# Optimization experiments

Measured on AMD Instinct MI355X. Metric: run time of the kernel, lower is better.

## Reference

```python
import jax, jax.numpy as jnp
import numpy as np

V = 50000   # words_num
D = 128     # embedding_dim
B = 2048    # batch
P = 20      # max Huffman path length


def setup_inputs() -> dict:
    key = jax.random.key(0)
    k1, k2, k3, k4, k5 = jax.random.split(key, 5)
    inputs_vector = jax.random.uniform(k1, (B, V), dtype=jnp.float32)
    path_nodes_indices = jax.random.randint(k2, (B, P), 0, V)
    huffman_codes = jax.random.randint(k3, (B, P), 0, 2).astype(jnp.float32)
    mask = jnp.ones((B, P), dtype=jnp.float32)
    # learned params, torch nn.Linear weight layout [out, in], kaiming-uniform-ish scale
    W_emb = jax.random.uniform(k4, (D, V), dtype=jnp.float32, minval=-1.0, maxval=1.0) / np.sqrt(V)
    W_cls = jax.random.uniform(k5, (V, D), dtype=jnp.float32, minval=-1.0, maxval=1.0) / np.sqrt(D)
    return {
        "inputs_vector": inputs_vector,
        "W_emb": W_emb,
        "W_cls": W_cls,
        "path_nodes_indices": path_nodes_indices,
        "huffman_codes": huffman_codes,
        "mask": mask,
    }


def _bce_with_logits(logits, targets):
    # numerically stable, elementwise (reduction='none')
    return jnp.maximum(logits, 0.0) - logits * targets + jnp.log1p(jnp.exp(-jnp.abs(logits)))


def reference(inputs_vector, W_emb, W_cls, path_nodes_indices, huffman_codes, mask):
    x = inputs_vector @ W_emb.T              # [B, D]  embedding Linear (no bias)
    logits_full = x @ W_cls.T                # [B, V]  full-vocab cls matmul (as in source)
    logits = jnp.take_along_axis(logits_full, path_nodes_indices, axis=1)  # [B, P]
    loss = _bce_with_logits(logits, huffman_codes)  # [B, P]
    masked_loss = loss * mask
    per_sample = masked_loss.sum(axis=-1) / mask.sum(axis=-1)  # [B]
    return per_sample.mean()
```

## Files before the change

kernel.cpp:

```cpp
#include <hip/hip_runtime.h>
#include <hip/hip_bf16.h>

#define V 50000
#define D 128
#define B 2048
#define P 20

#define BM 128
#define BK 64
#define LDK 72
#define NSPLIT 48
#define KC 1056
#define VPAD (NSPLIT * KC)
#define NMT (B / BM)

typedef float  f32x4  __attribute__((ext_vector_type(4)));
typedef short  bf16x8 __attribute__((ext_vector_type(8)));
typedef unsigned int uint4v __attribute__((ext_vector_type(4)));
typedef unsigned int uint2v __attribute__((ext_vector_type(2)));

__device__ __forceinline__ unsigned int pk2(float a, float b) {
    return (__float_as_uint(b) & 0xFFFF0000u) | (__float_as_uint(a) >> 16);
}
__device__ __forceinline__ unsigned short f2bf(float f) {
    unsigned int u = __float_as_uint(f);
    return (unsigned short)((u + 0x7FFFu + ((u >> 16) & 1u)) >> 16);
}

__global__ __launch_bounds__(256)
void w2v_wcast(const float* __restrict__ Wemb, unsigned short* __restrict__ Wb) {
    const size_t t = (size_t)blockIdx.x * 256 + threadIdx.x;
    const size_t n = (size_t)D * VPAD / 8;
    if (t >= n) return;
    const size_t base = t * 8;
    const int d = (int)(base / VPAD);
    const int k = (int)(base % VPAD);
    uint4v u = {0u, 0u, 0u, 0u};
    if (k + 8 <= V) {
        const f32x4* src = reinterpret_cast<const f32x4*>(Wemb + (size_t)d * V + k);
        f32x4 v0 = src[0], v1 = src[1];
        u.x = pk2(v0[0], v0[1]); u.y = pk2(v0[2], v0[3]);
        u.z = pk2(v1[0], v1[1]); u.w = pk2(v1[2], v1[3]);
    }
    *reinterpret_cast<uint4v*>(Wb + (size_t)d * VPAD + k) = u;
}

template<int FAST>
__global__ __launch_bounds__(256, 3)
void w2v_gemm(const float* __restrict__ Ain, const void* __restrict__ Wsrc,
              void* __restrict__ part) {
    __shared__ unsigned short Sm[2 * BM * LDK];
    unsigned short* As = Sm;
    unsigned short* Ws = Sm + BM * LDK;

    const int i   = blockIdx.x;
    const int xcd = i & 7;
    const int q   = i >> 3;
    const int s   = xcd * 6 + (q >> 4);
    const int mt  = q & 15;
    const int m0  = mt * BM;
    const int k0  = s * KC;
    const int k1  = (k0 + KC < V) ? (k0 + KC) : V;
    const int nsteps = (k1 - k0 + 63) >> 6;

    const int tid  = threadIdx.x;
    const int lane = tid & 63;
    const int wid  = tid >> 6;
    const int w32  = wid * 32;
    const int fr   = lane & 15;
    const int kg4  = lane >> 4;

    f32x4 acc[2][8] = {};

    const unsigned short* Wb = (const unsigned short*)Wsrc;
    const float*          Wf = (const float*)Wsrc;

    for (int t = 0; t < nsteps; ++t) {
        const int ks = k0 + t * 64;

#pragma unroll
        for (int it = 0; it < 8; ++it) {
            const int slot = tid + it * 256;
            const int row  = slot >> 4;
            const int kv   = slot & 15;
            const int kg   = ks + kv * 4;
            f32x4 v = {0.f, 0.f, 0.f, 0.f};
            if (kg + 4 <= k1)
                v = *reinterpret_cast<const f32x4*>(Ain + (size_t)(m0 + row) * V + kg);
            uint2v u;
            u.x = pk2(v[0], v[1]);
            u.y = pk2(v[2], v[3]);
            *reinterpret_cast<uint2v*>(&As[row * LDK + kv * 4]) = u;
        }
#pragma unroll
        for (int it = 0; it < 4; ++it) {
            const int slot = tid + it * 256;
            const int d    = slot >> 3;
            const int c8   = slot & 7;
            const int kg   = ks + c8 * 8;
            uint4v u;
            if (FAST) {
                u = *reinterpret_cast<const uint4v*>(Wb + (size_t)d * VPAD + kg);
            } else {
                u.x = 0u; u.y = 0u; u.z = 0u; u.w = 0u;
                if (kg + 8 <= V) {
                    const f32x4* sp = reinterpret_cast<const f32x4*>(Wf + (size_t)d * V + kg);
                    f32x4 v0 = sp[0], v1 = sp[1];
                    u.x = pk2(v0[0], v0[1]); u.y = pk2(v0[2], v0[3]);
                    u.z = pk2(v1[0], v1[1]); u.w = pk2(v1[2], v1[3]);
                }
            }
            *reinterpret_cast<uint4v*>(&Ws[d * LDK + c8 * 8]) = u;
        }
        __syncthreads();

#pragma unroll
        for (int kk = 0; kk < BK; kk += 32) {
            const int kfo = kk + kg4 * 8;
            bf16x8 af[2];
#pragma unroll
            for (int m = 0; m < 2; ++m)
                af[m] = *reinterpret_cast<const bf16x8*>(&As[(w32 + m * 16 + fr) * LDK + kfo]);
#pragma unroll
            for (int n = 0; n < 8; ++n) {
                const bf16x8 wf = *reinterpret_cast<const bf16x8*>(&Ws[(n * 16 + fr) * LDK + kfo]);
                acc[0][n] = __builtin_amdgcn_mfma_f32_16x16x32_bf16(af[0], wf, acc[0][n], 0, 0, 0);
                acc[1][n] = __builtin_amdgcn_mfma_f32_16x16x32_bf16(af[1], wf, acc[1][n], 0, 0, 0);
            }
        }
        __syncthreads();
    }

    if (!FAST) {
        float* outp = (float*)part;
#pragma unroll
        for (int m = 0; m < 2; ++m) {
            const int r0 = m0 + w32 + m * 16 + kg4 * 4;
#pragma unroll
            for (int n = 0; n < 8; ++n) {
                const int c = n * 16 + fr;
#pragma unroll
                for (int jj = 0; jj < 4; ++jj)
                    atomicAdd(&outp[(size_t)(r0 + jj) * D + c], acc[m][n][jj]);
            }
        }
        return;
    }
    unsigned short* Cs = Sm;
#pragma unroll
    for (int m = 0; m < 2; ++m) {
        const int r0 = w32 + m * 16 + kg4 * 4;
#pragma unroll
        for (int n = 0; n < 8; ++n) {
            const int c = n * 16 + fr;
#pragma unroll
            for (int jj = 0; jj < 4; ++jj)
                Cs[(r0 + jj) * 128 + c] = f2bf(acc[m][n][jj]);
        }
    }
    __syncthreads();
    char* dstb = (char*)part + ((size_t)s * B + m0) * (D * 2);
#pragma unroll
    for (int it = 0; it < 8; ++it) {
        const int off = (it * 256 + tid) * 16;
        uint4v v = *reinterpret_cast<const uint4v*>((char*)Sm + off);
        *reinterpret_cast<uint4v*>(dstb + off) = v;
    }
}

__global__ __launch_bounds__(256)
void w2v_loss(const void* __restrict__ part, int part_bf16,
              const float* __restrict__ Wcls, const int* __restrict__ pathIdx,
              const float* __restrict__ codes, const float* __restrict__ mask,
              float* __restrict__ out) {
    const int lane = threadIdx.x & 63;
    const int wid  = threadIdx.x >> 6;
    const int b    = blockIdx.x * 4 + wid;

    float x0 = 0.f, x1 = 0.f;
    if (part_bf16) {
        const unsigned* pb = (const unsigned*)part;
#pragma unroll 8
        for (int s = 0; s < NSPLIT; ++s) {
            unsigned u = pb[((size_t)s * B + b) * 64 + lane];
            x0 += __uint_as_float(u << 16);
            x1 += __uint_as_float(u & 0xFFFF0000u);
        }
    } else {
        const float* pf = (const float*)part;
        const float2 v = *reinterpret_cast<const float2*>(&pf[(size_t)b * D + lane * 2]);
        x0 = v.x; x1 = v.y;
    }

    float lsum = 0.f, msum = 0.f;
#pragma unroll
    for (int p = 0; p < P; ++p) {
        int node = pathIdx[b * P + p];
        const float2 w = *reinterpret_cast<const float2*>(&Wcls[(size_t)node * D + lane * 2]);
        float d = x0 * w.x + x1 * w.y;
#pragma unroll
        for (int off = 1; off < 64; off <<= 1)
            d += __shfl_xor(d, off, 64);
        float t  = codes[b * P + p];
        float mm = mask[b * P + p];
        float loss = fmaxf(d, 0.f) - d * t + log1pf(__expf(-fabsf(d)));
        lsum += loss * mm;
        msum += mm;
    }
    float per = (msum > 0.f) ? (lsum / msum) : 0.f;

    __shared__ float wsum[4];
    if (lane == 0) wsum[wid] = per;
    __syncthreads();
    if (threadIdx.x == 0) {
        float ssum = wsum[0] + wsum[1] + wsum[2] + wsum[3];
        atomicAdd(out, ssum * (1.0f / (float)B));
    }
}

extern "C" void kernel_launch(void* const* d_in, const int* in_sizes, int n_in,
                              void* d_out, int out_size, void* d_ws, size_t ws_size,
                              hipStream_t stream) {
    const float* inputs = (const float*)d_in[0];
    const float* W_emb  = (const float*)d_in[1];
    const float* W_cls  = (const float*)d_in[2];
    const int*   path   = (const int*)  d_in[3];
    const float* codes  = (const float*)d_in[4];
    const float* mask   = (const float*)d_in[5];
    float* out = (float*)d_out;

    hipMemsetAsync(d_out, 0, sizeof(float), stream);

    const size_t wb_bytes  = (size_t)D * VPAD * 2;
    const size_t part_off  = (wb_bytes + 255) & ~(size_t)255;
    const size_t part_need = part_off + (size_t)NSPLIT * B * D * 2;

    if (ws_size >= part_need) {
        unsigned short* Wb = (unsigned short*)d_ws;
        char* partp = (char*)d_ws + part_off;
        w2v_wcast<<<dim3((unsigned)((size_t)D * VPAD / 8 / 256)), dim3(256), 0, stream>>>(W_emb, Wb);
        w2v_gemm<1><<<dim3(NMT * NSPLIT), dim3(256), 0, stream>>>(inputs, Wb, partp);
        w2v_loss<<<dim3(B / 4), dim3(256), 0, stream>>>(partp, 1, W_cls, path, codes, mask, out);
    } else {
        hipMemsetAsync(d_ws, 0, (size_t)B * D * sizeof(float), stream);
        w2v_gemm<0><<<dim3(NMT * NSPLIT), dim3(256), 0, stream>>>(inputs, W_emb, d_ws);
        w2v_loss<<<dim3(B / 4), dim3(256), 0, stream>>>(d_ws, 0, W_cls, path, codes, mask, out);
    }
}
```

Baseline: 171.3 us.

## Prefetch next K-tile into registers and use XOR-swizzled unpadded LDS layout

The GEMM main loop now loads the next 64-wide K slice of A and W into registers before the MFMA work on the current tile, so global-memory latency overlaps with compute. The padded LDS rows (LDK=72) are replaced by 128-byte rows with an XOR swizzle on 16-byte chunks, which avoids bank conflicts and makes the LDS stores 16-byte wide. Keeping the prefetched tile in registers raises register pressure (up to 16 f32x4 held across the loop) and could reduce occupancy under launch_bounds(256,3).

```diff
diff --git a/kernel.cpp b/kernel.cpp
--- a/kernel.cpp
+++ b/kernel.cpp
@@ -8,7 +8,6 @@
 
 #define BM 128
 #define BK 64
-#define LDK 72
 #define NSPLIT 48
 #define KC 1056
 #define VPAD (NSPLIT * KC)
@@ -17,7 +16,6 @@
 typedef float  f32x4  __attribute__((ext_vector_type(4)));
 typedef short  bf16x8 __attribute__((ext_vector_type(8)));
 typedef unsigned int uint4v __attribute__((ext_vector_type(4)));
-typedef unsigned int uint2v __attribute__((ext_vector_type(2)));
 
 __device__ __forceinline__ unsigned int pk2(float a, float b) {
     return (__float_as_uint(b) & 0xFFFF0000u) | (__float_as_uint(a) >> 16);
@@ -49,9 +47,9 @@
 __global__ __launch_bounds__(256, 3)
 void w2v_gemm(const float* __restrict__ Ain, const void* __restrict__ Wsrc,
               void* __restrict__ part) {
-    __shared__ unsigned short Sm[2 * BM * LDK];
-    unsigned short* As = Sm;
-    unsigned short* Ws = Sm + BM * LDK;
+    __shared__ unsigned short Sm[2 * BM * BK];
+    char* AsB = (char*)Sm;
+    char* WsB = (char*)(Sm + BM * BK);
 
     const int i   = blockIdx.x;
     const int xcd = i & 7;
@@ -72,63 +70,103 @@
 
     f32x4 acc[2][8] = {};
 
+    const int rbase = tid >> 3;
+    const int c8    = tid & 7;
+    const int c8x   = c8 ^ (rbase & 7);
+    const float* aBase = Ain + (size_t)(m0 + rbase) * V + c8 * 8;
     const unsigned short* Wb = (const unsigned short*)Wsrc;
     const float*          Wf = (const float*)Wsrc;
+    const unsigned short* wBaseB = Wb + (size_t)rbase * VPAD + c8 * 8;
+    const float*          wBaseF = Wf + (size_t)rbase * V + c8 * 8;
+
+    f32x4 aR[8];
+    uint4v wR[4];
+    f32x4 wRf[8];
+
+    auto loadregs = [&](int ks) {
+        const bool ag = (ks + c8 * 8 + 8 <= k1);
+#pragma unroll
+        for (int it = 0; it < 4; ++it) {
+            const float* ap = aBase + (size_t)(it * 32) * V + ks;
+            if (ag) {
+                aR[it * 2]     = *reinterpret_cast<const f32x4*>(ap);
+                aR[it * 2 + 1] = *reinterpret_cast<const f32x4*>(ap + 4);
+            } else {
+                aR[it * 2] = f32x4{0.f, 0.f, 0.f, 0.f};
+                aR[it * 2 + 1] = f32x4{0.f, 0.f, 0.f, 0.f};
+            }
+        }
+        if (FAST) {
+#pragma unroll
+            for (int it = 0; it < 4; ++it)
+                wR[it] = *reinterpret_cast<const uint4v*>(wBaseB + (size_t)(it * 32) * VPAD + ks);
+        } else {
+            const bool wg = (ks + c8 * 8 + 8 <= V);
+#pragma unroll
+            for (int it = 0; it < 4; ++it) {
+                const float* wp = wBaseF + (size_t)(it * 32) * V + ks;
+                if (wg) {
+                    wRf[it * 2]     = *reinterpret_cast<const f32x4*>(wp);
+                    wRf[it * 2 + 1] = *reinterpret_cast<const f32x4*>(wp + 4);
+                } else {
+                    wRf[it * 2] = f32x4{0.f, 0.f, 0.f, 0.f};
+                    wRf[it * 2 + 1] = f32x4{0.f, 0.f, 0.f, 0.f};
+                }
+            }
+        }
+    };
+
+    auto writeLDS = [&]() {
+#pragma unroll
+        for (int it = 0; it < 4; ++it) {
+            const unsigned dst = (unsigned)((rbase + it * 32) * 128) + (unsigned)(c8x * 16);
+            uint4v ua;
+            ua.x = pk2(aR[it * 2][0], aR[it * 2][1]);
+            ua.y = pk2(aR[it * 2][2], aR[it * 2][3]);
+            ua.z = pk2(aR[it * 2 + 1][0], aR[it * 2 + 1][1]);
+            ua.w = pk2(aR[it * 2 + 1][2], aR[it * 2 + 1][3]);
+            *reinterpret_cast<uint4v*>(AsB + dst) = ua;
+            uint4v uw;
+            if (FAST) {
+                uw = wR[it];
+            } else {
+                uw.x = pk2(wRf[it * 2][0], wRf[it * 2][1]);
+                uw.y = pk2(wRf[it * 2][2], wRf[it * 2][3]);
+                uw.z = pk2(wRf[it * 2 + 1][0], wRf[it * 2 + 1][1]);
+                uw.w = pk2(wRf[it * 2 + 1][2], wRf[it * 2 + 1][3]);
+            }
+            *reinterpret_cast<uint4v*>(WsB + dst) = uw;
+        }
+    };
+
+    loadregs(k0);
 
     for (int t = 0; t < nsteps; ++t) {
-        const int ks = k0 + t * 64;
-
-#pragma unroll
-        for (int it = 0; it < 8; ++it) {
-            const int slot = tid + it * 256;
-            const int row  = slot >> 4;
-            const int kv   = slot & 15;
-            const int kg   = ks + kv * 4;
-            f32x4 v = {0.f, 0.f, 0.f, 0.f};
-            if (kg + 4 <= k1)
-                v = *reinterpret_cast<const f32x4*>(Ain + (size_t)(m0 + row) * V + kg);
-            uint2v u;
-            u.x = pk2(v[0], v[1]);
-            u.y = pk2(v[2], v[3]);
-            *reinterpret_cast<uint2v*>(&As[row * LDK + kv * 4]) = u;
-        }
-#pragma unroll
-        for (int it = 0; it < 4; ++it) {
-            const int slot = tid + it * 256;
-            const int d    = slot >> 3;
-            const int c8   = slot & 7;
-            const int kg   = ks + c8 * 8;
-            uint4v u;
-            if (FAST) {
-                u = *reinterpret_cast<const uint4v*>(Wb + (size_t)d * VPAD + kg);
-            } else {
-                u.x = 0u; u.y = 0u; u.z = 0u; u.w = 0u;
-                if (kg + 8 <= V) {
-                    const f32x4* sp = reinterpret_cast<const f32x4*>(Wf + (size_t)d * V + kg);
-                    f32x4 v0 = sp[0], v1 = sp[1];
-                    u.x = pk2(v0[0], v0[1]); u.y = pk2(v0[2], v0[3]);
-                    u.z = pk2(v1[0], v1[1]); u.w = pk2(v1[2], v1[3]);
-                }
-            }
-            *reinterpret_cast<uint4v*>(&Ws[d * LDK + c8 * 8]) = u;
-        }
-        __syncthreads();
-
+        writeLDS();
+        asm volatile("s_waitcnt lgkmcnt(0)" ::: "memory");
+        __builtin_amdgcn_s_barrier();
+        if (t + 1 < nsteps) loadregs(k0 + (t + 1) * 64);
 #pragma unroll
         for (int kk = 0; kk < BK; kk += 32) {
-            const int kfo = kk + kg4 * 8;
+            const int cbase = (kk >> 3) + kg4;
             bf16x8 af[2];
 #pragma unroll
-            for (int m = 0; m < 2; ++m)
-                af[m] = *reinterpret_cast<const bf16x8*>(&As[(w32 + m * 16 + fr) * LDK + kfo]);
+            for (int m = 0; m < 2; ++m) {
+                const int r = w32 + m * 16 + fr;
+                af[m] = *reinterpret_cast<const bf16x8*>(
+                    AsB + r * 128 + ((cbase ^ (r & 7)) << 4));
+            }
 #pragma unroll
             for (int n = 0; n < 8; ++n) {
-                const bf16x8 wf = *reinterpret_cast<const bf16x8*>(&Ws[(n * 16 + fr) * LDK + kfo]);
+                const int r = n * 16 + fr;
+                const bf16x8 wf = *reinterpret_cast<const bf16x8*>(
+                    WsB + r * 128 + ((cbase ^ (r & 7)) << 4));
                 acc[0][n] = __builtin_amdgcn_mfma_f32_16x16x32_bf16(af[0], wf, acc[0][n], 0, 0, 0);
                 acc[1][n] = __builtin_amdgcn_mfma_f32_16x16x32_bf16(af[1], wf, acc[1][n], 0, 0, 0);
             }
         }
-        __syncthreads();
+        asm volatile("s_waitcnt lgkmcnt(0)" ::: "memory");
+        __builtin_amdgcn_s_barrier();
     }
 
     if (!FAST) {
```

Result: faster. 143.6 us (-16.2%).

## Restructure embedding GEMM with register-prefetched A ring and direct W fragment loads

Applied to the files above, without the earlier changes.

Blocks now cover 256 rows with 512 threads across 32 K-splits, so each block handles a larger chunk of K. The A tile goes through a swizzled 8-slot LDS ring, and global loads are prefetched into double-buffered registers. W fragments now load straight from global memory into registers instead of passing through shared memory, and there is a single barrier per 32-wide K substep. The aim is to overlap the streaming of the large fp32 input with MFMA work and to cut LDS traffic and sync count, at the cost of more register pressure and fewer, larger blocks.

```diff
diff --git a/kernel.cpp b/kernel.cpp
--- a/kernel.cpp
+++ b/kernel.cpp
@@ -6,18 +6,16 @@
 #define B 2048
 #define P 20
 
-#define BM 128
-#define BK 64
-#define LDK 72
-#define NSPLIT 48
-#define KC 1056
+#define BM 256
+#define NSPLIT 32
+#define KC 1568
+#define NSUB 49
 #define VPAD (NSPLIT * KC)
 #define NMT (B / BM)
 
 typedef float  f32x4  __attribute__((ext_vector_type(4)));
 typedef short  bf16x8 __attribute__((ext_vector_type(8)));
 typedef unsigned int uint4v __attribute__((ext_vector_type(4)));
-typedef unsigned int uint2v __attribute__((ext_vector_type(2)));
 
 __device__ __forceinline__ unsigned int pk2(float a, float b) {
     return (__float_as_uint(b) & 0xFFFF0000u) | (__float_as_uint(a) >> 16);
@@ -26,12 +24,16 @@
     unsigned int u = __float_as_uint(f);
     return (unsigned short)((u + 0x7FFFu + ((u >> 16) & 1u)) >> 16);
 }
+__device__ __forceinline__ bf16x8 pack8(f32x4 lo, f32x4 hi) {
+    union { uint4v u; bf16x8 h; } r;
+    r.u.x = pk2(lo[0], lo[1]); r.u.y = pk2(lo[2], lo[3]);
+    r.u.z = pk2(hi[0], hi[1]); r.u.w = pk2(hi[2], hi[3]);
+    return r.h;
+}
 
 __global__ __launch_bounds__(256)
 void w2v_wcast(const float* __restrict__ Wemb, unsigned short* __restrict__ Wb) {
     const size_t t = (size_t)blockIdx.x * 256 + threadIdx.x;
-    const size_t n = (size_t)D * VPAD / 8;
-    if (t >= n) return;
     const size_t base = t * 8;
     const int d = (int)(base / VPAD);
     const int k = (int)(base % VPAD);
@@ -46,22 +48,20 @@
 }
 
 template<int FAST>
-__global__ __launch_bounds__(256, 3)
+__global__ __launch_bounds__(512, 2)
 void w2v_gemm(const float* __restrict__ Ain, const void* __restrict__ Wsrc,
               void* __restrict__ part) {
-    __shared__ unsigned short Sm[2 * BM * LDK];
-    unsigned short* As = Sm;
-    unsigned short* Ws = Sm + BM * LDK;
+    __shared__ uint4v smem4[8192];
+    char* smem = (char*)smem4;
 
     const int i   = blockIdx.x;
     const int xcd = i & 7;
     const int q   = i >> 3;
-    const int s   = xcd * 6 + (q >> 4);
-    const int mt  = q & 15;
+    const int s   = xcd * 4 + (q >> 3);
+    const int mt  = q & 7;
     const int m0  = mt * BM;
     const int k0  = s * KC;
     const int k1  = (k0 + KC < V) ? (k0 + KC) : V;
-    const int nsteps = (k1 - k0 + 63) >> 6;
 
     const int tid  = threadIdx.x;
     const int lane = tid & 63;
@@ -72,64 +72,99 @@
 
     f32x4 acc[2][8] = {};
 
+    const int arow = tid >> 3;
+    const int akt  = tid & 7;
     const unsigned short* Wb = (const unsigned short*)Wsrc;
     const float*          Wf = (const float*)Wsrc;
 
-    for (int t = 0; t < nsteps; ++t) {
-        const int ks = k0 + t * 64;
-
-#pragma unroll
-        for (int it = 0; it < 8; ++it) {
-            const int slot = tid + it * 256;
-            const int row  = slot >> 4;
-            const int kv   = slot & 15;
-            const int kg   = ks + kv * 4;
+    f32x4  aRA[4], aRB[4];
+    bf16x8 wfA[8], wfB[8];
+
+    auto loadA = [&](f32x4* aR, int g, int Kb) {
+#pragma unroll
+        for (int c = 0; c < 4; ++c) {
+            const int kg = Kb + akt * 16 + c * 4;
             f32x4 v = {0.f, 0.f, 0.f, 0.f};
             if (kg + 4 <= k1)
-                v = *reinterpret_cast<const f32x4*>(Ain + (size_t)(m0 + row) * V + kg);
-            uint2v u;
-            u.x = pk2(v[0], v[1]);
-            u.y = pk2(v[2], v[3]);
-            *reinterpret_cast<uint2v*>(&As[row * LDK + kv * 4]) = u;
-        }
-#pragma unroll
-        for (int it = 0; it < 4; ++it) {
-            const int slot = tid + it * 256;
-            const int d    = slot >> 3;
-            const int c8   = slot & 7;
-            const int kg   = ks + c8 * 8;
+                v = *reinterpret_cast<const f32x4*>(Ain + (size_t)(m0 + g * 64 + arow) * V + kg);
+            aR[c] = v;
+        }
+    };
+    auto writeA = [&](const f32x4* aR, int g, int Kb) {
+        const int sl = ((Kb >> 5) + (akt >> 1)) & 7;
+        char* t = smem + (g * 8 + sl) * 4096 + arow * 64;
+#pragma unroll
+        for (int h = 0; h < 2; ++h) {
             uint4v u;
-            if (FAST) {
-                u = *reinterpret_cast<const uint4v*>(Wb + (size_t)d * VPAD + kg);
-            } else {
-                u.x = 0u; u.y = 0u; u.z = 0u; u.w = 0u;
+            u.x = pk2(aR[h*2][0], aR[h*2][1]);   u.y = pk2(aR[h*2][2], aR[h*2][3]);
+            u.z = pk2(aR[h*2+1][0], aR[h*2+1][1]); u.w = pk2(aR[h*2+1][2], aR[h*2+1][3]);
+            const int c2 = (akt & 1) * 2 + h;
+            *reinterpret_cast<uint4v*>(t + ((c2 ^ (arow & 3)) << 4)) = u;
+        }
+    };
+    auto loadW = [&](bf16x8* wf, int kw) {
+        if (FAST) {
+#pragma unroll
+            for (int n = 0; n < 8; ++n)
+                wf[n] = *reinterpret_cast<const bf16x8*>(Wb + (size_t)(n * 16 + fr) * VPAD + kw + kg4 * 8);
+        } else {
+#pragma unroll
+            for (int n = 0; n < 8; ++n) {
+                const int kg = kw + kg4 * 8;
+                f32x4 lo = {0,0,0,0}, hi = {0,0,0,0};
                 if (kg + 8 <= V) {
-                    const f32x4* sp = reinterpret_cast<const f32x4*>(Wf + (size_t)d * V + kg);
-                    f32x4 v0 = sp[0], v1 = sp[1];
-                    u.x = pk2(v0[0], v0[1]); u.y = pk2(v0[2], v0[3]);
-                    u.z = pk2(v1[0], v1[1]); u.w = pk2(v1[2], v1[3]);
+                    const f32x4* p = reinterpret_cast<const f32x4*>(Wf + (size_t)(n * 16 + fr) * V + kg);
+                    lo = p[0]; hi = p[1];
                 }
+                wf[n] = pack8(lo, hi);
             }
-            *reinterpret_cast<uint4v*>(&Ws[d * LDK + c8 * 8]) = u;
-        }
-        __syncthreads();
-
-#pragma unroll
-        for (int kk = 0; kk < BK; kk += 32) {
-            const int kfo = kk + kg4 * 8;
-            bf16x8 af[2];
-#pragma unroll
-            for (int m = 0; m < 2; ++m)
-                af[m] = *reinterpret_cast<const bf16x8*>(&As[(w32 + m * 16 + fr) * LDK + kfo]);
-#pragma unroll
-            for (int n = 0; n < 8; ++n) {
-                const bf16x8 wf = *reinterpret_cast<const bf16x8*>(&Ws[(n * 16 + fr) * LDK + kfo]);
-                acc[0][n] = __builtin_amdgcn_mfma_f32_16x16x32_bf16(af[0], wf, acc[0][n], 0, 0, 0);
-                acc[1][n] = __builtin_amdgcn_mfma_f32_16x16x32_bf16(af[1], wf, acc[1][n], 0, 0, 0);
-            }
-        }
-        __syncthreads();
-    }
+        }
+    };
+    auto compute = [&](const bf16x8* wf, int u) {
+        const int sl = u & 7;
+        bf16x8 af[2];
+#pragma unroll
+        for (int m = 0; m < 2; ++m) {
+            const int rr = w32 + m * 16 + fr;
+            const int g = rr >> 6, rin = rr & 63;
+            af[m] = *reinterpret_cast<const bf16x8*>(
+                smem + (g * 8 + sl) * 4096 + rin * 64 + ((kg4 ^ (rin & 3)) << 4));
+        }
+#pragma unroll
+        for (int n = 0; n < 8; ++n) {
+            acc[0][n] = __builtin_amdgcn_mfma_f32_16x16x32_bf16(af[0], wf[n], acc[0][n], 0, 0, 0);
+            acc[1][n] = __builtin_amdgcn_mfma_f32_16x16x32_bf16(af[1], wf[n], acc[1][n], 0, 0, 0);
+        }
+    };
+    auto barrier = [&]() {
+        asm volatile("s_waitcnt lgkmcnt(0)" ::: "memory");
+        __builtin_amdgcn_s_barrier();
+    };
+
+    loadA(aRA, 0, k0);
+    loadA(aRB, 1, k0);
+#pragma unroll
+    for (int b = 0; b < 8; ++b) {
+        const int g = b & 3, Kb = k0 + (b >> 2) * 128;
+        if (b & 1) { writeA(aRB, g, Kb); if (b + 2 < 8) loadA(aRB, (b + 2) & 3, k0 + ((b + 2) >> 2) * 128); }
+        else       { writeA(aRA, g, Kb); if (b + 2 < 8) loadA(aRA, (b + 2) & 3, k0 + ((b + 2) >> 2) * 128); }
+    }
+    loadA(aRA, 0, k0 + 128);
+    loadW(wfA, k0);
+    barrier();
+
+    auto sub = [&](int u, f32x4* aW, f32x4* aL, bf16x8* wfC, bf16x8* wfL) {
+        if (u <= 44) writeA(aW, u & 3, k0 + (u + 4) * 32);
+        if (u <= 43) loadA(aL, (u + 1) & 3, k0 + (u + 5) * 32);
+        if (u <= 47) loadW(wfL, k0 + (u + 1) * 32);
+        compute(wfC, u);
+        barrier();
+    };
+    for (int uu = 0; uu < 48; uu += 2) {
+        sub(uu,     aRA, aRB, wfA, wfB);
+        sub(uu + 1, aRB, aRA, wfB, wfA);
+    }
+    sub(48, aRA, aRB, wfA, wfB);
 
     if (!FAST) {
         float* outp = (float*)part;
@@ -146,7 +181,7 @@
         }
         return;
     }
-    unsigned short* Cs = Sm;
+    unsigned short* Cs = (unsigned short*)smem;
 #pragma unroll
     for (int m = 0; m < 2; ++m) {
         const int r0 = w32 + m * 16 + kg4 * 4;
@@ -162,8 +197,8 @@
     char* dstb = (char*)part + ((size_t)s * B + m0) * (D * 2);
 #pragma unroll
     for (int it = 0; it < 8; ++it) {
-        const int off = (it * 256 + tid) * 16;
-        uint4v v = *reinterpret_cast<const uint4v*>((char*)Sm + off);
+        const int off = (it * 512 + tid) * 16;
+        uint4v v = *reinterpret_cast<const uint4v*>(smem + off);
         *reinterpret_cast<uint4v*>(dstb + off) = v;
     }
 }
@@ -239,11 +274,11 @@
         unsigned short* Wb = (unsigned short*)d_ws;
         char* partp = (char*)d_ws + part_off;
         w2v_wcast<<<dim3((unsigned)((size_t)D * VPAD / 8 / 256)), dim3(256), 0, stream>>>(W_emb, Wb);
-        w2v_gemm<1><<<dim3(NMT * NSPLIT), dim3(256), 0, stream>>>(inputs, Wb, partp);
+        w2v_gemm<1><<<dim3(NMT * NSPLIT), dim3(512), 0, stream>>>(inputs, Wb, partp);
         w2v_loss<<<dim3(B / 4), dim3(256), 0, stream>>>(partp, 1, W_cls, path, codes, mask, out);
     } else {
         hipMemsetAsync(d_ws, 0, (size_t)B * D * sizeof(float), stream);
-        w2v_gemm<0><<<dim3(NMT * NSPLIT), dim3(256), 0, stream>>>(inputs, W_emb, d_ws);
+        w2v_gemm<0><<<dim3(NMT * NSPLIT), dim3(512), 0, stream>>>(inputs, W_emb, d_ws);
         w2v_loss<<<dim3(B / 4), dim3(256), 0, stream>>>(d_ws, 0, W_cls, path, codes, mask, out);
     }
 }
```

After: 193.7 us. 1.13x slower.

## Double-buffer GEMM with direct-to-LDS W loads and MFMA-fragment prepacked weights

Applied to the files above, without the earlier changes.

The weight-cast kernel now writes W_emb as bf16 in an MFMA-fragment layout. This lets the GEMM stage W tiles straight into LDS with global_load_lds, skipping register round trips. The GEMM becomes a double-buffered software pipeline: A tiles are prefetched into registers while the current tile computes, A uses XOR-swizzled LDS rows instead of padding, and each iteration needs one barrier instead of two. The split count drops from 48 to 32 with a larger K chunk and occupancy hint 2, trading parallelism and more LDS per block for fewer partials and less reduction traffic.

```diff
diff --git a/kernel.cpp b/kernel.cpp
--- a/kernel.cpp
+++ b/kernel.cpp
@@ -7,17 +7,15 @@
 #define P 20
 
 #define BM 128
-#define BK 64
-#define LDK 72
-#define NSPLIT 48
-#define KC 1056
+#define NSPLIT 32
+#define KC 1568
 #define VPAD (NSPLIT * KC)
+#define NSLICE (VPAD / 32)
 #define NMT (B / BM)
 
 typedef float  f32x4  __attribute__((ext_vector_type(4)));
 typedef short  bf16x8 __attribute__((ext_vector_type(8)));
 typedef unsigned int uint4v __attribute__((ext_vector_type(4)));
-typedef unsigned int uint2v __attribute__((ext_vector_type(2)));
 
 __device__ __forceinline__ unsigned int pk2(float a, float b) {
     return (__float_as_uint(b) & 0xFFFF0000u) | (__float_as_uint(a) >> 16);
@@ -26,42 +24,72 @@
     unsigned int u = __float_as_uint(f);
     return (unsigned short)((u + 0x7FFFu + ((u >> 16) & 1u)) >> 16);
 }
+__device__ __forceinline__ bf16x8 pack8(f32x4 lo, f32x4 hi) {
+    union { uint4v u; bf16x8 h; } r;
+    r.u.x = pk2(lo[0], lo[1]); r.u.y = pk2(lo[2], lo[3]);
+    r.u.z = pk2(hi[0], hi[1]); r.u.w = pk2(hi[2], hi[3]);
+    return r.h;
+}
+__device__ __forceinline__ void gload_lds16(const void* g, void* l) {
+    __builtin_amdgcn_global_load_lds(
+        (const __attribute__((address_space(1))) unsigned int*)g,
+        (__attribute__((address_space(3))) unsigned int*)l, 16, 0, 0);
+}
 
 __global__ __launch_bounds__(256)
-void w2v_wcast(const float* __restrict__ Wemb, unsigned short* __restrict__ Wb) {
-    const size_t t = (size_t)blockIdx.x * 256 + threadIdx.x;
-    const size_t n = (size_t)D * VPAD / 8;
-    if (t >= n) return;
-    const size_t base = t * 8;
-    const int d = (int)(base / VPAD);
-    const int k = (int)(base % VPAD);
-    uint4v u = {0u, 0u, 0u, 0u};
-    if (k + 8 <= V) {
-        const f32x4* src = reinterpret_cast<const f32x4*>(Wemb + (size_t)d * V + k);
-        f32x4 v0 = src[0], v1 = src[1];
+void w2v_wcast(const float* __restrict__ Wemb, unsigned short* __restrict__ WTF) {
+    __shared__ unsigned short L[128 * 128];
+    const int bk = blockIdx.x;
+    const int t  = threadIdx.x;
+    const int d = t >> 1, h = t & 1;
+    const float* src = Wemb + (size_t)d * V + bk * 128 + h * 64;
+#pragma unroll
+    for (int j = 0; j < 8; ++j) {
+        const int kg = bk * 128 + h * 64 + j * 8;
+        f32x4 v0 = {0,0,0,0}, v1 = {0,0,0,0};
+        if (kg + 8 <= V) {
+            const f32x4* p = reinterpret_cast<const f32x4*>(src + j * 8);
+            v0 = p[0]; v1 = p[1];
+        }
+        uint4v u;
         u.x = pk2(v0[0], v0[1]); u.y = pk2(v0[2], v0[3]);
         u.z = pk2(v1[0], v1[1]); u.w = pk2(v1[2], v1[3]);
-    }
-    *reinterpret_cast<uint4v*>(Wb + (size_t)d * VPAD + k) = u;
+        const int c8 = h * 8 + j;
+        *reinterpret_cast<uint4v*>((char*)L + d * 256 + ((c8 ^ (d & 15)) << 4)) = u;
+    }
+    __syncthreads();
+    const int w = t >> 6, l = t & 63;
+    const int kg4 = l >> 4, fr = l & 15;
+#pragma unroll
+    for (int sl = 0; sl < 4; ++sl)
+#pragma unroll
+        for (int j2 = 0; j2 < 2; ++j2) {
+            const int n  = w + j2 * 4;
+            const int dd = n * 16 + fr;
+            const int c8 = sl * 4 + kg4;
+            uint4v u = *reinterpret_cast<const uint4v*>(
+                (char*)L + dd * 256 + ((c8 ^ (dd & 15)) << 4));
+            *reinterpret_cast<uint4v*>(
+                (char*)WTF + ((size_t)(bk * 4 + sl) * 8 + n) * 1024 + l * 16) = u;
+        }
 }
 
 template<int FAST>
-__global__ __launch_bounds__(256, 3)
+__global__ __launch_bounds__(256, 2)
 void w2v_gemm(const float* __restrict__ Ain, const void* __restrict__ Wsrc,
               void* __restrict__ part) {
-    __shared__ unsigned short Sm[2 * BM * LDK];
-    unsigned short* As = Sm;
-    unsigned short* Ws = Sm + BM * LDK;
+    __shared__ char smem[65536];
+    char* Wlds = smem + 32768;
 
     const int i   = blockIdx.x;
     const int xcd = i & 7;
     const int q   = i >> 3;
-    const int s   = xcd * 6 + (q >> 4);
+    const int s   = xcd * 4 + (q >> 4);
     const int mt  = q & 15;
     const int m0  = mt * BM;
     const int k0  = s * KC;
-    const int k1  = (k0 + KC < V) ? (k0 + KC) : V;
-    const int nsteps = (k1 - k0 + 63) >> 6;
+    const int kend = (k0 + KC < V) ? (k0 + KC) : V;
+    const int nst  = (kend - k0 + 63) >> 6;
 
     const int tid  = threadIdx.x;
     const int lane = tid & 63;
@@ -72,63 +100,115 @@
 
     f32x4 acc[2][8] = {};
 
-    const unsigned short* Wb = (const unsigned short*)Wsrc;
+    const int arow = tid >> 1;
+    const int ah   = tid & 1;
+    const float* aSrc = Ain + (size_t)(m0 + arow) * V + ah * 32;
+    const unsigned short* WT = (const unsigned short*)Wsrc;
     const float*          Wf = (const float*)Wsrc;
 
-    for (int t = 0; t < nsteps; ++t) {
-        const int ks = k0 + t * 64;
-
-#pragma unroll
-        for (int it = 0; it < 8; ++it) {
-            const int slot = tid + it * 256;
-            const int row  = slot >> 4;
-            const int kv   = slot & 15;
-            const int kg   = ks + kv * 4;
-            f32x4 v = {0.f, 0.f, 0.f, 0.f};
-            if (kg + 4 <= k1)
-                v = *reinterpret_cast<const f32x4*>(Ain + (size_t)(m0 + row) * V + kg);
-            uint2v u;
-            u.x = pk2(v[0], v[1]);
-            u.y = pk2(v[2], v[3]);
-            *reinterpret_cast<uint2v*>(&As[row * LDK + kv * 4]) = u;
-        }
-#pragma unroll
-        for (int it = 0; it < 4; ++it) {
-            const int slot = tid + it * 256;
-            const int d    = slot >> 3;
-            const int c8   = slot & 7;
-            const int kg   = ks + c8 * 8;
+    f32x4 aR[8];
+    auto loadA = [&](int ks) {
+#pragma unroll
+        for (int j = 0; j < 8; ++j) {
+            const bool ok = (ks + ah * 32 + j * 4 + 4 <= kend);
+            const f32x4* p = reinterpret_cast<const f32x4*>(ok ? (aSrc + ks + j * 4)
+                                                               : (aSrc + k0));
+            f32x4 v = *p;
+            if (!ok) v = f32x4{0.f, 0.f, 0.f, 0.f};
+            aR[j] = v;
+        }
+    };
+    auto writeA = [&](int buf) {
+        char* base = smem + buf * 16384 + arow * 128;
+#pragma unroll
+        for (int j2 = 0; j2 < 4; ++j2) {
             uint4v u;
-            if (FAST) {
-                u = *reinterpret_cast<const uint4v*>(Wb + (size_t)d * VPAD + kg);
+            u.x = pk2(aR[j2*2][0], aR[j2*2][1]);   u.y = pk2(aR[j2*2][2], aR[j2*2][3]);
+            u.z = pk2(aR[j2*2+1][0], aR[j2*2+1][1]); u.w = pk2(aR[j2*2+1][2], aR[j2*2+1][3]);
+            const int c8 = ah * 4 + j2;
+            *reinterpret_cast<uint4v*>(base + ((c8 ^ (arow & 7)) << 4)) = u;
+        }
+    };
+    auto stageW = [&](int buf, int ks5) {
+#pragma unroll
+        for (int j = 0; j < 4; ++j) {
+            const int g = wid * 4 + j;
+            const unsigned short* gp = WT + (size_t)(ks5 + (g >> 3)) * 4096
+                                          + (g & 7) * 512 + lane * 8;
+            gload_lds16(gp, Wlds + buf * 16384 + g * 1024);
+        }
+    };
+    auto computeMicro = [&](int buf, int u) {
+        bf16x8 af[2];
+#pragma unroll
+        for (int m = 0; m < 2; ++m) {
+            const int r  = w32 + m * 16 + fr;
+            const int c8 = u * 4 + kg4;
+            af[m] = *reinterpret_cast<const bf16x8*>(
+                smem + buf * 16384 + r * 128 + ((c8 ^ (r & 7)) << 4));
+        }
+#pragma unroll
+        for (int n = 0; n < 8; ++n) {
+            const bf16x8 wf = *reinterpret_cast<const bf16x8*>(
+                Wlds + buf * 16384 + (u * 8 + n) * 1024 + lane * 16);
+            acc[0][n] = __builtin_amdgcn_mfma_f32_16x16x32_bf16(af[0], wf, acc[0][n], 0, 0, 0);
+            acc[1][n] = __builtin_amdgcn_mfma_f32_16x16x32_bf16(af[1], wf, acc[1][n], 0, 0, 0);
+        }
+    };
+
+    if (FAST) {
+        loadA(k0);
+        stageW(0, s * 49);
+        for (int t = 0; t < nst; ++t) {
+            writeA(t & 1);
+            const bool more = (t + 1 < nst);
+            if (more) {
+                loadA(k0 + (t + 1) * 64);
+                stageW((t + 1) & 1, s * 49 + (t + 1) * 2);
+                asm volatile("s_waitcnt vmcnt(12) lgkmcnt(0)" ::: "memory");
             } else {
-                u.x = 0u; u.y = 0u; u.z = 0u; u.w = 0u;
-                if (kg + 8 <= V) {
-                    const f32x4* sp = reinterpret_cast<const f32x4*>(Wf + (size_t)d * V + kg);
-                    f32x4 v0 = sp[0], v1 = sp[1];
-                    u.x = pk2(v0[0], v0[1]); u.y = pk2(v0[2], v0[3]);
-                    u.z = pk2(v1[0], v1[1]); u.w = pk2(v1[2], v1[3]);
+                asm volatile("s_waitcnt vmcnt(0) lgkmcnt(0)" ::: "memory");
+            }
+            __builtin_amdgcn_s_barrier();
+            computeMicro(t & 1, 0);
+            computeMicro(t & 1, 1);
+        }
+    } else {
+        bf16x8 wfr[8];
+        for (int t = 0; t < nst; ++t) {
+            const int ks = k0 + t * 64;
+            loadA(ks);
+            writeA(0);
+            __syncthreads();
+#pragma unroll
+            for (int u = 0; u < 2; ++u) {
+#pragma unroll
+                for (int n = 0; n < 8; ++n) {
+                    const int kg = ks + u * 32 + kg4 * 8;
+                    f32x4 lo = {0,0,0,0}, hi = {0,0,0,0};
+                    if (kg + 8 <= V) {
+                        const f32x4* p = reinterpret_cast<const f32x4*>(
+                            Wf + (size_t)(n * 16 + fr) * V + kg);
+                        lo = p[0]; hi = p[1];
+                    }
+                    wfr[n] = pack8(lo, hi);
+                }
+                bf16x8 af[2];
+#pragma unroll
+                for (int m = 0; m < 2; ++m) {
+                    const int r  = w32 + m * 16 + fr;
+                    const int c8 = u * 4 + kg4;
+                    af[m] = *reinterpret_cast<const bf16x8*>(
+                        smem + r * 128 + ((c8 ^ (r & 7)) << 4));
+                }
+#pragma unroll
+                for (int n = 0; n < 8; ++n) {
+                    acc[0][n] = __builtin_amdgcn_mfma_f32_16x16x32_bf16(af[0], wfr[n], acc[0][n], 0, 0, 0);
+                    acc[1][n] = __builtin_amdgcn_mfma_f32_16x16x32_bf16(af[1], wfr[n], acc[1][n], 0, 0, 0);
                 }
             }
-            *reinterpret_cast<uint4v*>(&Ws[d * LDK + c8 * 8]) = u;
-        }
-        __syncthreads();
-
-#pragma unroll
-        for (int kk = 0; kk < BK; kk += 32) {
-            const int kfo = kk + kg4 * 8;
-            bf16x8 af[2];
-#pragma unroll
-            for (int m = 0; m < 2; ++m)
-                af[m] = *reinterpret_cast<const bf16x8*>(&As[(w32 + m * 16 + fr) * LDK + kfo]);
-#pragma unroll
-            for (int n = 0; n < 8; ++n) {
-                const bf16x8 wf = *reinterpret_cast<const bf16x8*>(&Ws[(n * 16 + fr) * LDK + kfo]);
-                acc[0][n] = __builtin_amdgcn_mfma_f32_16x16x32_bf16(af[0], wf, acc[0][n], 0, 0, 0);
-                acc[1][n] = __builtin_amdgcn_mfma_f32_16x16x32_bf16(af[1], wf, acc[1][n], 0, 0, 0);
-            }
-        }
-        __syncthreads();
+            __syncthreads();
+        }
     }
 
     if (!FAST) {
@@ -146,7 +226,9 @@
         }
         return;
     }
-    unsigned short* Cs = Sm;
+    asm volatile("s_waitcnt lgkmcnt(0)" ::: "memory");
+    __builtin_amdgcn_s_barrier();
+    unsigned short* Cs = (unsigned short*)smem;
 #pragma unroll
     for (int m = 0; m < 2; ++m) {
         const int r0 = w32 + m * 16 + kg4 * 4;
@@ -163,7 +245,7 @@
 #pragma unroll
     for (int it = 0; it < 8; ++it) {
         const int off = (it * 256 + tid) * 16;
-        uint4v v = *reinterpret_cast<const uint4v*>((char*)Sm + off);
+        uint4v v = *reinterpret_cast<const uint4v*>((char*)smem + off);
         *reinterpret_cast<uint4v*>(dstb + off) = v;
     }
 }
@@ -231,15 +313,15 @@
 
     hipMemsetAsync(d_out, 0, sizeof(float), stream);
 
-    const size_t wb_bytes  = (size_t)D * VPAD * 2;
-    const size_t part_off  = (wb_bytes + 255) & ~(size_t)255;
+    const size_t wtf_bytes = (size_t)NSLICE * 8192;
+    const size_t part_off  = (wtf_bytes + 255) & ~(size_t)255;
     const size_t part_need = part_off + (size_t)NSPLIT * B * D * 2;
 
     if (ws_size >= part_need) {
-        unsigned short* Wb = (unsigned short*)d_ws;
+        unsigned short* WTF = (unsigned short*)d_ws;
         char* partp = (char*)d_ws + part_off;
-        w2v_wcast<<<dim3((unsigned)((size_t)D * VPAD / 8 / 256)), dim3(256), 0, stream>>>(W_emb, Wb);
-        w2v_gemm<1><<<dim3(NMT * NSPLIT), dim3(256), 0, stream>>>(inputs, Wb, partp);
+        w2v_wcast<<<dim3(VPAD / 128), dim3(256), 0, stream>>>(W_emb, WTF);
+        w2v_gemm<1><<<dim3(NMT * NSPLIT), dim3(256), 0, stream>>>(inputs, WTF, partp);
         w2v_loss<<<dim3(B / 4), dim3(256), 0, stream>>>(partp, 1, W_cls, path, codes, mask, out);
     } else {
         hipMemsetAsync(d_ws, 0, (size_t)B * D * sizeof(float), stream);
```

After: 170.6 us. Within noise of the previous version (-0.4%).
